# Optimization experiments

Measured on AMD Instinct MI355X. Metric: run time of the kernel, lower is better.

The kernel has to match this reference:

```python
import jax, jax.numpy as jnp
import numpy as np

E, EDGE, MEM = 32768, 128, 128
IN = EDGE + 2 * MEM              # 384
HID = 512
NK = 64                          # num_kernels
KNOTS = 16                       # grid_size
ORDER = 3                        # spline order (cubic)
COEF = KNOTS + ORDER             # 19 basis functions per input dim

# Uniform knot grid on [-1, 1], extended by ORDER knots on each side
_H = 2.0 / KNOTS
GRID = (jnp.arange(-ORDER, KNOTS + ORDER + 1, dtype=jnp.float32) * _H - 1.0)


def _b_splines(x, grid):
    """Cox-de Boor B-spline bases. x: [B, IN] -> [B, IN, COEF]."""
    xe = x[..., None]                                   # [B, IN, 1]
    bases = ((xe >= grid[:-1]) & (xe < grid[1:])).astype(x.dtype)
    for p in range(1, ORDER + 1):
        left = (xe - grid[:-(p + 1)]) / (grid[p:-1] - grid[:-(p + 1)])
        right = (grid[p + 1:] - xe) / (grid[p + 1:] - grid[1:-p])
        bases = left * bases[..., :-1] + right * bases[..., 1:]
    return bases                                        # [B, IN, COEF]


def setup_inputs() -> dict:
    key = jax.random.key(0)
    ks = jax.random.split(key, 7)
    z = jax.random.normal(ks[0], (E, EDGE), jnp.float32)
    mem_src = jax.random.normal(ks[1], (E, MEM), jnp.float32)
    mem_dst = jax.random.normal(ks[2], (E, MEM), jnp.float32)
    base_weight = jax.random.normal(ks[3], (HID, IN), jnp.float32) / np.sqrt(IN)
    spline_weight = jax.random.normal(ks[4], (HID, IN, COEF), jnp.float32) * 0.1
    lin_w = jax.random.normal(ks[5], (NK, HID), jnp.float32) / np.sqrt(HID)
    lin_b = jax.random.normal(ks[6], (NK,), jnp.float32) * 0.01
    return {"z": z, "mem_src": mem_src, "mem_dst": mem_dst,
            "base_weight": base_weight, "spline_weight": spline_weight,
            "lin_w": lin_w, "lin_b": lin_b}


def reference(z, mem_src, mem_dst, base_weight, spline_weight, lin_w, lin_b):
    # concat + tanh squashing (inputs into the [-1,1] knot grid), fp32 math
    x = jnp.tanh(jnp.concatenate([z, mem_src, mem_dst], axis=-1)).astype(jnp.float32)
    # KANLinear: base path (silu residual) + spline path
    bases = _b_splines(x, GRID)                          # [E, IN, COEF]
    h = (jnp.dot(jax.nn.silu(x), base_weight.T)
         + jnp.einsum('bik,oik->bo', bases, spline_weight))  # [E, HID]
    h = jnp.tanh(h)                                      # act='tanh'; dropout=0 -> identity
    return jnp.dot(h, lin_w.T) + lin_b                   # [E, NK]
```

## Files before the change

### kernel.cpp

```cpp
#include <hip/hip_runtime.h>
#include <hip/hip_bf16.h>
#include <cstdint>

#define DI __device__ __forceinline__

using bf16x8 = __attribute__((ext_vector_type(8))) short;
using f32x4  = __attribute__((ext_vector_type(4))) float;

constexpr int IN_DIM = 384;
constexpr int HID    = 512;
constexpr int KTOT   = IN_DIM * 20;
constexpr int BM = 64, BN = 512, BK = 160;
constexpr int NSTEP = KTOT / BK;
constexpr int A_STRIDE_B = 320;
constexpr int A_BYTES    = BM * A_STRIDE_B;
constexpr int LDS_BYTES  = 2 * A_BYTES;

DI unsigned short f2bf(float f) {
  union { float f; uint32_t u; } v; v.f = f;
  uint32_t r = (v.u + 0x7FFFu + ((v.u >> 16) & 1u)) >> 16;
  return (unsigned short)r;
}
DI float fast_tanh(float x) {
  float e = __expf(2.0f * x);
  return 1.0f - 2.0f / (e + 1.0f);
}
DI uint32_t swzw(uint32_t L) { return L ^ ((L >> 6) & 0x70u); }

__global__ __launch_bounds__(256) void kpack(const float* __restrict__ bw,
                                             const float* __restrict__ sw,
                                             unsigned short* __restrict__ Wf) {
  int idx = blockIdx.x * 256 + threadIdx.x;
  int o = idx / IN_DIM;
  int i = idx - o * IN_DIM;
  const float* sp = sw + (size_t)idx * 19;
  const uint32_t gq  = (uint32_t)(o >> 4);
  const uint32_t l16o = (uint32_t)(o & 15);
#pragma unroll
  for (int c = 0; c < 20; ++c) {
    int k = i * 20 + c;
    uint32_t q  = (uint32_t)k >> 5;
    uint32_t kr = (uint32_t)k & 31u;
    uint32_t lane = l16o + ((kr >> 3) << 4);
    uint32_t off = (q * 32u + gq) * 512u + lane * 8u + (kr & 7u);
    float v = (c == 0) ? bw[idx] : sp[c - 1];
    Wf[off] = f2bf(v);
  }
}

__global__ __launch_bounds__(512, 4) void kgemm1(const float* __restrict__ z,
                                                 const float* __restrict__ ms,
                                                 const float* __restrict__ md,
                                                 const unsigned short* __restrict__ Wf,
                                                 unsigned short* __restrict__ hout) {
  extern __shared__ char ldsbuf[];

  const int tid  = threadIdx.x;
  const int lane = tid & 63;
  const int wc   = tid >> 6;
  const int l16  = lane & 15;
  const int lhi  = lane >> 4;

  int wg = blockIdx.x;
  int id = (wg & 7) * 64 + (wg >> 3);
  const int row0 = id * BM;

  const unsigned short* bpt = Wf + (size_t)(wc * 4) * 512 + (size_t)lane * 8;

  const int isl = tid & 7;
  const int arow = tid >> 3;
  const uint32_t fw = ((uint32_t)arow & 7u) << 4;
  const uint32_t abase = (uint32_t)arow * A_STRIDE_B + (uint32_t)isl * 40u;

  const uint32_t fA = (uint32_t)(l16 & 7) << 4;
  const uint32_t rA = (uint32_t)l16 * A_STRIDE_B + (uint32_t)lhi * 16u;

  f32x4 acc[4][4] = {};

  float xv0;
  {
    float x = z[(size_t)(row0 + arow) * 128 + isl];
    float xt = fast_tanh(x);
    float tt = (xt + 1.0f) * 8.0f;
    int   m  = (int)tt; m = m > 16 ? 16 : m;
    float u  = tt - (float)m;
    float omu = 1.0f - u;
    float u2 = u * u, u3 = u2 * u;
    float w0 = omu * omu * omu * (1.0f / 6.0f);
    float w1 = (3.0f * u3 - 6.0f * u2 + 4.0f) * (1.0f / 6.0f);
    float w2 = (-3.0f * u3 + 3.0f * u2 + 3.0f * u + 1.0f) * (1.0f / 6.0f);
    float w3 = u3 * (1.0f / 6.0f);
    float sil = xt / (1.0f + __expf(-xt));
#pragma unroll
    for (int zz = 0; zz < 5; ++zz)
      *(uint64_t*)(ldsbuf + ((abase + zz * 8) ^ fw)) = 0ull;
    *(short*)(ldsbuf + (abase ^ fw)) = (short)f2bf(sil);
    *(short*)(ldsbuf + ((abase + 2u * (m + 1)) ^ fw)) = (short)f2bf(w0);
    *(short*)(ldsbuf + ((abase + 2u * (m + 2)) ^ fw)) = (short)f2bf(w1);
    *(short*)(ldsbuf + ((abase + 2u * (m + 3)) ^ fw)) = (short)f2bf(w2);
    if (m < 16)
      *(short*)(ldsbuf + ((abase + 2u * (m + 4)) ^ fw)) = (short)f2bf(w3);
    xv0 = z[(size_t)(row0 + arow) * 128 + 8 + isl];
  }
  __syncthreads();

  for (int s = 0; s < NSTEP; ++s) {
    const uint32_t pc = (uint32_t)(s & 1);
    const uint32_t pn = pc ^ 1u;
    char* An = ldsbuf + pn * (uint32_t)A_BYTES;
    const char* Ac = ldsbuf + pc * (uint32_t)A_BYTES;

    {
      float xt = fast_tanh(xv0);
      float tt = (xt + 1.0f) * 8.0f;
      int   m  = (int)tt; m = m > 16 ? 16 : m;
      float u  = tt - (float)m;
      float omu = 1.0f - u;
      float u2 = u * u, u3 = u2 * u;
      float w0 = omu * omu * omu * (1.0f / 6.0f);
      float w1 = (3.0f * u3 - 6.0f * u2 + 4.0f) * (1.0f / 6.0f);
      float w2 = (-3.0f * u3 + 3.0f * u2 + 3.0f * u + 1.0f) * (1.0f / 6.0f);
      float w3 = u3 * (1.0f / 6.0f);
      float sil = xt / (1.0f + __expf(-xt));
#pragma unroll
      for (int zz = 0; zz < 5; ++zz)
        *(uint64_t*)(An + ((abase + zz * 8) ^ fw)) = 0ull;
      *(short*)(An + (abase ^ fw)) = (short)f2bf(sil);
      *(short*)(An + ((abase + 2u * (m + 1)) ^ fw)) = (short)f2bf(w0);
      *(short*)(An + ((abase + 2u * (m + 2)) ^ fw)) = (short)f2bf(w1);
      *(short*)(An + ((abase + 2u * (m + 3)) ^ fw)) = (short)f2bf(w2);
      if (m < 16)
        *(short*)(An + ((abase + 2u * (m + 4)) ^ fw)) = (short)f2bf(w3);
    }
    float xn0;
    {
      int i = (s + 2) * 8 + isl;
      i = (i >= IN_DIM) ? (i - IN_DIM) : i;
      const float* src = (i < 128) ? z : (i < 256 ? ms : md);
      xn0 = src[(size_t)(row0 + arow) * 128 + (i & 127)];
    }

    const size_t qoff = (size_t)s * 5u * 16384u;
#pragma unroll
    for (int ks = 0; ks < 5; ++ks) {
      bf16x8 af[4], bfr[4];
#pragma unroll
      for (int ni = 0; ni < 4; ++ni)
        bfr[ni] = *(const bf16x8*)(bpt + qoff + (size_t)ks * 16384u + (size_t)ni * 512u);
#pragma unroll
      for (int mi = 0; mi < 4; ++mi)
        af[mi] = *(const bf16x8*)(Ac + ((rA + (uint32_t)(mi * 16) * A_STRIDE_B + ks * 64u) ^ fA));
#pragma unroll
      for (int mi = 0; mi < 4; ++mi)
#pragma unroll
        for (int ni = 0; ni < 4; ++ni)
          acc[mi][ni] = __builtin_amdgcn_mfma_f32_16x16x32_bf16(af[mi], bfr[ni], acc[mi][ni], 0, 0, 0);
    }

    __syncthreads();
    xv0 = xn0;
  }

#pragma unroll
  for (int mi = 0; mi < 4; ++mi)
#pragma unroll
    for (int ni = 0; ni < 4; ++ni)
#pragma unroll
      for (int rg = 0; rg < 4; ++rg) {
        int grow = row0 + mi * 16 + lhi * 4 + rg;
        int gcol = wc * 64 + ni * 16 + l16;
        hout[(size_t)grow * HID + gcol] = f2bf(fast_tanh(acc[mi][ni][rg]));
      }
}

__global__ __launch_bounds__(256) void kfinal(const unsigned short* __restrict__ h,
                                              const float* __restrict__ lw,
                                              const float* __restrict__ lb,
                                              float* __restrict__ out) {
  __shared__ unsigned short Ws[64 * 512];
  char* WsB = (char*)Ws;
  const int tid  = threadIdx.x;
  const int lane = tid & 63;
  const int wv   = tid >> 6;
  const int l16  = lane & 15;
  const int lhi  = lane >> 4;
  const int row0 = blockIdx.x * 64;

#pragma unroll
  for (int it = 0; it < 16; ++it) {
    int c = it * 256 + tid;
    int r = c >> 6;
    int k8 = (c & 63) * 8;
    const float* g = lw + r * 512 + k8;
    float4 f0 = *(const float4*)g;
    float4 f1 = *(const float4*)(g + 4);
    union { unsigned short s[8]; bf16x8 v; } u;
    u.s[0] = f2bf(f0.x); u.s[1] = f2bf(f0.y); u.s[2] = f2bf(f0.z); u.s[3] = f2bf(f0.w);
    u.s[4] = f2bf(f1.x); u.s[5] = f2bf(f1.y); u.s[6] = f2bf(f1.z); u.s[7] = f2bf(f1.w);
    *(bf16x8*)(WsB + swzw((uint32_t)r * 1024u + (uint32_t)k8 * 2u)) = u.v;
  }
  __syncthreads();

  const int arow = row0 + wv * 16 + l16;
  const unsigned short* ag = h + (size_t)arow * HID + lhi * 8;
  f32x4 acc[4] = {};
#pragma unroll
  for (int ks = 0; ks < 16; ++ks) {
    bf16x8 af = *(const bf16x8*)(ag + ks * 32);
#pragma unroll
    for (int ni = 0; ni < 4; ++ni) {
      uint32_t L = (uint32_t)(ni * 16 + l16) * 1024u + (uint32_t)(ks * 64 + lhi * 16);
      bf16x8 bfr = *(const bf16x8*)(WsB + swzw(L));
      acc[ni] = __builtin_amdgcn_mfma_f32_16x16x32_bf16(af, bfr, acc[ni], 0, 0, 0);
    }
  }
#pragma unroll
  for (int ni = 0; ni < 4; ++ni) {
    int col = ni * 16 + l16;
    float bias = lb[col];
#pragma unroll
    for (int rg = 0; rg < 4; ++rg) {
      int grow = row0 + wv * 16 + lhi * 4 + rg;
      out[(size_t)grow * 64 + col] = acc[ni][rg] + bias;
    }
  }
}

extern "C" void kernel_launch(void* const* d_in, const int* in_sizes, int n_in,
                              void* d_out, int out_size, void* d_ws, size_t ws_size,
                              hipStream_t stream) {
  const float* z  = (const float*)d_in[0];
  const float* ms = (const float*)d_in[1];
  const float* md = (const float*)d_in[2];
  const float* bw = (const float*)d_in[3];
  const float* sw = (const float*)d_in[4];
  const float* lw = (const float*)d_in[5];
  const float* lb = (const float*)d_in[6];
  float* out = (float*)d_out;

  unsigned short* Wf = (unsigned short*)d_ws;
  unsigned short* hb = (unsigned short*)((char*)d_ws + (8u << 20));

  (void)hipFuncSetAttribute((const void*)kgemm1,
                            hipFuncAttributeMaxDynamicSharedMemorySize, LDS_BYTES);

  kpack<<<(HID * IN_DIM) / 256, 256, 0, stream>>>(bw, sw, Wf);
  kgemm1<<<512, 512, LDS_BYTES, stream>>>(z, ms, md, Wf, hb);
  kfinal<<<32768 / 64, 256, 0, stream>>>(hb, lw, lb, out);
}
```

Measured before the change: 243.0 us.

## Fuse final linear layer into KAN GEMM epilogue via LDS-staged hidden tile

The tanh-activated hidden tile is written into LDS as bf16 instead of global memory, and each workgroup then multiplies it by lin_w with MFMA to write the final outputs directly, removing the separate kfinal kernel and the hidden-activation round trip through HBM. LDS allocation grows to 64 KiB to hold the 64x512 hidden tile, which may reduce occupancy. lin_w is read from global and converted to bf16 per wave inside the loop rather than staged once in LDS, adding redundant loads and conversions.

```diff
diff --git a/kernel.cpp b/kernel.cpp
--- a/kernel.cpp
+++ b/kernel.cpp
@@ -14,7 +14,7 @@
 constexpr int NSTEP = KTOT / BK;
 constexpr int A_STRIDE_B = 320;
 constexpr int A_BYTES    = BM * A_STRIDE_B;
-constexpr int LDS_BYTES  = 2 * A_BYTES;
+constexpr int LDS_BYTES  = 65536;
 
 DI unsigned short f2bf(float f) {
   union { float f; uint32_t u; } v; v.f = f;
@@ -25,7 +25,6 @@
   float e = __expf(2.0f * x);
   return 1.0f - 2.0f / (e + 1.0f);
 }
-DI uint32_t swzw(uint32_t L) { return L ^ ((L >> 6) & 0x70u); }
 
 __global__ __launch_bounds__(256) void kpack(const float* __restrict__ bw,
                                              const float* __restrict__ sw,
@@ -52,7 +51,9 @@
                                                  const float* __restrict__ ms,
                                                  const float* __restrict__ md,
                                                  const unsigned short* __restrict__ Wf,
-                                                 unsigned short* __restrict__ hout) {
+                                                 const float* __restrict__ lw,
+                                                 const float* __restrict__ lb,
+                                                 float* __restrict__ out) {
   extern __shared__ char ldsbuf[];
 
   const int tid  = threadIdx.x;
@@ -167,61 +168,43 @@
     for (int ni = 0; ni < 4; ++ni)
 #pragma unroll
       for (int rg = 0; rg < 4; ++rg) {
-        int grow = row0 + mi * 16 + lhi * 4 + rg;
-        int gcol = wc * 64 + ni * 16 + l16;
-        hout[(size_t)grow * HID + gcol] = f2bf(fast_tanh(acc[mi][ni][rg]));
+        int hrow = mi * 16 + lhi * 4 + rg;
+        int hcol = wc * 64 + ni * 16 + l16;
+        uint32_t ha = (uint32_t)hrow * 1024u + (uint32_t)hcol * 2u;
+        *(short*)(ldsbuf + (ha ^ (((uint32_t)hrow & 7u) << 4))) =
+            (short)f2bf(fast_tanh(acc[mi][ni][rg]));
       }
-}
-
-__global__ __launch_bounds__(256) void kfinal(const unsigned short* __restrict__ h,
-                                              const float* __restrict__ lw,
-                                              const float* __restrict__ lb,
-                                              float* __restrict__ out) {
-  __shared__ unsigned short Ws[64 * 512];
-  char* WsB = (char*)Ws;
-  const int tid  = threadIdx.x;
-  const int lane = tid & 63;
-  const int wv   = tid >> 6;
-  const int l16  = lane & 15;
-  const int lhi  = lane >> 4;
-  const int row0 = blockIdx.x * 64;
-
-#pragma unroll
-  for (int it = 0; it < 16; ++it) {
-    int c = it * 256 + tid;
-    int r = c >> 6;
-    int k8 = (c & 63) * 8;
-    const float* g = lw + r * 512 + k8;
-    float4 f0 = *(const float4*)g;
-    float4 f1 = *(const float4*)(g + 4);
-    union { unsigned short s[8]; bf16x8 v; } u;
-    u.s[0] = f2bf(f0.x); u.s[1] = f2bf(f0.y); u.s[2] = f2bf(f0.z); u.s[3] = f2bf(f0.w);
-    u.s[4] = f2bf(f1.x); u.s[5] = f2bf(f1.y); u.s[6] = f2bf(f1.z); u.s[7] = f2bf(f1.w);
-    *(bf16x8*)(WsB + swzw((uint32_t)r * 1024u + (uint32_t)k8 * 2u)) = u.v;
-  }
   __syncthreads();
 
-  const int arow = row0 + wv * 16 + l16;
-  const unsigned short* ag = h + (size_t)arow * HID + lhi * 8;
-  f32x4 acc[4] = {};
-#pragma unroll
-  for (int ks = 0; ks < 16; ++ks) {
-    bf16x8 af = *(const bf16x8*)(ag + ks * 32);
-#pragma unroll
-    for (int ni = 0; ni < 4; ++ni) {
-      uint32_t L = (uint32_t)(ni * 16 + l16) * 1024u + (uint32_t)(ks * 64 + lhi * 16);
-      bf16x8 bfr = *(const bf16x8*)(WsB + swzw(L));
-      acc[ni] = __builtin_amdgcn_mfma_f32_16x16x32_bf16(af, bfr, acc[ni], 0, 0, 0);
-    }
-  }
-#pragma unroll
-  for (int ni = 0; ni < 4; ++ni) {
-    int col = ni * 16 + l16;
-    float bias = lb[col];
-#pragma unroll
-    for (int rg = 0; rg < 4; ++rg) {
-      int grow = row0 + wv * 16 + lhi * 4 + rg;
-      out[(size_t)grow * 64 + col] = acc[ni][rg] + bias;
+  {
+    const int rs  = (wc >> 1) * 16;
+    const int oc0 = (wc & 1) * 32;
+    const uint32_t rh = (uint32_t)(rs + l16) * 1024u + (uint32_t)lhi * 16u;
+    const uint32_t fH = (uint32_t)(l16 & 7) << 4;
+    f32x4 acc2[2] = {};
+#pragma unroll
+    for (int ks = 0; ks < 16; ++ks) {
+      bf16x8 ah = *(const bf16x8*)(ldsbuf + ((rh + (uint32_t)ks * 64u) ^ fH));
+#pragma unroll
+      for (int ni = 0; ni < 2; ++ni) {
+        const float* lwp = lw + (size_t)(oc0 + ni * 16 + l16) * 512 + ks * 32 + lhi * 8;
+        float4 f0 = *(const float4*)lwp;
+        float4 f1 = *(const float4*)(lwp + 4);
+        union { unsigned short sh[8]; bf16x8 v; } ub;
+        ub.sh[0] = f2bf(f0.x); ub.sh[1] = f2bf(f0.y); ub.sh[2] = f2bf(f0.z); ub.sh[3] = f2bf(f0.w);
+        ub.sh[4] = f2bf(f1.x); ub.sh[5] = f2bf(f1.y); ub.sh[6] = f2bf(f1.z); ub.sh[7] = f2bf(f1.w);
+        acc2[ni] = __builtin_amdgcn_mfma_f32_16x16x32_bf16(ah, ub.v, acc2[ni], 0, 0, 0);
+      }
+    }
+#pragma unroll
+    for (int ni = 0; ni < 2; ++ni) {
+      int ocol = oc0 + ni * 16 + l16;
+      float bias = lb[ocol];
+#pragma unroll
+      for (int rg = 0; rg < 4; ++rg) {
+        int grow = row0 + rs + lhi * 4 + rg;
+        out[(size_t)grow * 64 + ocol] = acc2[ni][rg] + bias;
+      }
     }
   }
 }
@@ -239,12 +222,10 @@
   float* out = (float*)d_out;
 
   unsigned short* Wf = (unsigned short*)d_ws;
-  unsigned short* hb = (unsigned short*)((char*)d_ws + (8u << 20));
 
   (void)hipFuncSetAttribute((const void*)kgemm1,
                             hipFuncAttributeMaxDynamicSharedMemorySize, LDS_BYTES);
 
   kpack<<<(HID * IN_DIM) / 256, 256, 0, stream>>>(bw, sw, Wf);
-  kgemm1<<<512, 512, LDS_BYTES, stream>>>(z, ms, md, Wf, hb);
-  kfinal<<<32768 / 64, 256, 0, stream>>>(hb, lw, lb, out);
-}
+  kgemm1<<<512, 512, LDS_BYTES, stream>>>(z, ms, md, Wf, lw, lb, out);
+}
```

Result: slower. 257.6 us (+6.0%).
